# Performance work log

Measured on AMD Instinct MI355X. Metric: run time of the kernel, lower is better.

The kernel has to match this reference:

```python
import jax, jax.numpy as jnp
import numpy as np
import math

B, L = 32, 1000
N_CHAR, EMB, D_MODEL, N_HEADS, PRED_HS, N_OUT = 256, 512, 512, 8, 512, 8
D_HEAD = D_MODEL // N_HEADS


def _pos_encoding(seq_len, d_model, dtype=jnp.float32):
    pos = jnp.arange(seq_len, dtype=dtype)[:, None]                      # [L,1]
    div = jnp.exp(jnp.arange(0, d_model, 2, dtype=dtype) * (-math.log(10000.0) / d_model))
    pe = jnp.zeros((seq_len, d_model), dtype=dtype)
    pe = pe.at[:, 0::2].set(jnp.sin(pos * div))
    pe = pe.at[:, 1::2].set(jnp.cos(pos * div))
    return pe                                                            # [L,D]


def setup_inputs() -> dict:
    key = jax.random.key(0)
    ks = jax.random.split(key, 12)
    def xavier(k, shape):
        fan_in, fan_out = shape[1], shape[0]
        lim = math.sqrt(6.0 / (fan_in + fan_out))
        return jax.random.uniform(k, shape, jnp.float32, -lim, lim)
    data = jax.random.randint(ks[0], (B, L), 0, N_CHAR, dtype=jnp.int64)
    lengths = jnp.clip(jax.random.randint(ks[1], (B,), 0, L, dtype=jnp.int64), 1, L)
    emb = jax.random.normal(ks[2], (N_CHAR, EMB), jnp.float32) * math.sqrt(2.0 / (N_CHAR + EMB))
    return {
        'data': data,
        'lengths': lengths,
        'emb': emb,
        'Wq': xavier(ks[3], (D_MODEL, EMB)), 'bq': jnp.zeros((D_MODEL,), jnp.float32),
        'Wk': xavier(ks[4], (D_MODEL, EMB)), 'bk': jnp.zeros((D_MODEL,), jnp.float32),
        'Wv': xavier(ks[5], (D_MODEL, EMB)), 'bv': jnp.zeros((D_MODEL,), jnp.float32),
        'W1': xavier(ks[6], (PRED_HS, D_MODEL)), 'b1': jnp.full((PRED_HS,), 0.01, jnp.float32),
        'W2': xavier(ks[7], (N_OUT, PRED_HS)), 'b2': jnp.full((N_OUT,), 0.01, jnp.float32),
    }


def reference(data, lengths, emb, Wq, bq, Wk, bk, Wv, bv, W1, b1, W2, b2):
    bs, seq = data.shape
    x = emb[data]                                              # [B,L,E]
    x = x + _pos_encoding(seq, x.shape[-1], x.dtype)[None]     # positional encoding
    # q/k/v projections -> [B,L,H,dh]
    q = (x @ Wq.T + bq).reshape(bs, seq, N_HEADS, D_HEAD)
    k = (x @ Wk.T + bk).reshape(bs, seq, N_HEADS, D_HEAD)
    v = (x @ Wv.T + bv).reshape(bs, seq, N_HEADS, D_HEAD)
    scale = 1.0 / math.sqrt(D_HEAD)
    score = jnp.einsum('bqhd,bkhd->bhqk', q, k) * scale        # [B,H,L,L]
    causal = jnp.tril(jnp.ones((seq, seq), dtype=bool))        # True = keep
    score = jnp.where(causal[None, None], score, -jnp.inf)
    attn = jax.nn.softmax(score, axis=-1)
    ctx = jnp.einsum('bhqk,bkhd->bqhd', attn, v).reshape(bs, seq, D_MODEL)
    # take hidden state at last valid position per sequence
    ctx_last = jnp.take_along_axis(ctx, (lengths - 1)[:, None, None].astype(jnp.int32), axis=1)[:, 0]  # [B,D]
    h = jax.nn.leaky_relu(ctx_last @ W1.T + b1)                # pred layer 1
    out = jax.nn.relu(h @ W2.T + b2)                           # [B,8]
    out = jnp.mean(out, axis=-1)                               # [B]
    return jax.nn.leaky_relu(out)
```

## Files before the change

### kernel.cpp

```cpp
#include <hip/hip_runtime.h>
#include <math.h>

#define BATCH   32
#define LSEQ    1000
#define LPAD    1024
#define NHEADS  8
#define DHEAD   64

__device__ __forceinline__ unsigned short f2bf(float f) {
  unsigned u = __builtin_bit_cast(unsigned, f);
  u += 0x7fffu + ((u >> 16) & 1u);
  return (unsigned short)(u >> 16);
}
__device__ __forceinline__ float bf2f(unsigned short h) {
  return __builtin_bit_cast(float, ((unsigned)h) << 16);
}

__global__ __launch_bounds__(256) void build_x_kernel(
    const int* __restrict__ data, const int* __restrict__ lengths,
    const float* __restrict__ emb, unsigned short* __restrict__ X) {
  int t    = threadIdx.x;
  int row  = blockIdx.x * 4 + (t >> 6);
  int b    = row / 1000;
  int j    = row - b * 1000;
  int p    = lengths[b] - 1;
  if (j > p) return;
  int lane = t & 63;
  int e0   = lane * 8;
  int tok  = data[row];
  const float* ev = emb + (size_t)tok * 512 + e0;
  float4 a = *(const float4*)(ev);
  float4 c = *(const float4*)(ev + 4);
  float vals[8] = {a.x, a.y, a.z, a.w, c.x, c.y, c.z, c.w};
  #pragma unroll
  for (int i = 0; i < 8; i += 2) {
    int e = e0 + i;
    float dv  = __expf((float)e * (-9.210340371976184f / 512.0f));
    float arg = (float)j * dv;
    vals[i]     += __sinf(arg);
    vals[i + 1] += __cosf(arg);
  }
  unsigned w0 = (unsigned)f2bf(vals[0]) | ((unsigned)f2bf(vals[1]) << 16);
  unsigned w1 = (unsigned)f2bf(vals[2]) | ((unsigned)f2bf(vals[3]) << 16);
  unsigned w2 = (unsigned)f2bf(vals[4]) | ((unsigned)f2bf(vals[5]) << 16);
  unsigned w3 = (unsigned)f2bf(vals[6]) | ((unsigned)f2bf(vals[7]) << 16);
  uint4 pk; pk.x = w0; pk.y = w1; pk.z = w2; pk.w = w3;
  *(uint4*)(X + ((size_t)(b * LPAD + j)) * 512 + e0) = pk;
}

__global__ __launch_bounds__(256) void qfold_kernel(
    const unsigned short* __restrict__ X, const int* __restrict__ lengths,
    const float* __restrict__ Wq, const float* __restrict__ bq,
    const float* __restrict__ Wk, const float* __restrict__ bk,
    float* __restrict__ wfold, float* __restrict__ bias_dot) {
  int h = blockIdx.x, b = blockIdx.y;
  int p = lengths[b] - 1;
  int t = threadIdx.x;
  __shared__ float xs[512];
  __shared__ float red[256];
  __shared__ float qs[64];
  const unsigned short* xr = X + ((size_t)(b * LPAD + p)) * 512;
  xs[t]       = bf2f(xr[t]);
  xs[t + 256] = bf2f(xr[t + 256]);
  __syncthreads();
  int col = h * 64 + (t & 63);
  int kp  = t >> 6;
  {
    const float* wr = Wq + (size_t)col * 512 + kp * 128;
    const float* xp = xs + kp * 128;
    float a = 0.0f;
    for (int e = 0; e < 128; e += 4) {
      float4 wv = *(const float4*)(wr + e);
      a += wv.x * xp[e] + wv.y * xp[e + 1] + wv.z * xp[e + 2] + wv.w * xp[e + 3];
    }
    red[t] = a;
  }
  __syncthreads();
  if (t < 64) {
    float qval = (red[t] + red[t + 64] + red[t + 128] + red[t + 192]
                  + bq[h * 64 + t]) * 0.125f;
    qs[t] = qval;
    float bd = qval * bk[h * 64 + t];
    #pragma unroll
    for (int o = 32; o > 0; o >>= 1) bd += __shfl_xor(bd, o, 64);
    if (t == 0) bias_dot[b * NHEADS + h] = bd;
  }
  __syncthreads();
  float a0 = 0.0f, a1 = 0.0f;
  const float* wkb = Wk + (size_t)(h * 64) * 512;
  for (int d = 0; d < 64; ++d) {
    float qd = qs[d];
    a0 += qd * wkb[d * 512 + t];
    a1 += qd * wkb[d * 512 + t + 256];
  }
  size_t wb = ((size_t)(b * NHEADS + h)) * 512;
  wfold[wb + t]       = a0;
  wfold[wb + t + 256] = a1;
}

__global__ __launch_bounds__(256) void score_kernel(
    const unsigned short* __restrict__ X, const float* __restrict__ wfold,
    const float* __restrict__ bias_dot, const int* __restrict__ lengths,
    float* __restrict__ scores) {
  int b = blockIdx.y;
  int n_keys = lengths[b];
  int row0 = blockIdx.x * 16;
  if (row0 >= n_keys) return;
  int t = threadIdx.x;
  int w = t >> 6, lane = t & 63;
  float wf[8][8];
  float bd[8];
  size_t wbase = ((size_t)b * NHEADS) * 512 + lane * 8;
  #pragma unroll
  for (int h = 0; h < 8; ++h) {
    float4 u0 = *(const float4*)(wfold + wbase + h * 512);
    float4 u1 = *(const float4*)(wfold + wbase + h * 512 + 4);
    wf[h][0] = u0.x; wf[h][1] = u0.y; wf[h][2] = u0.z; wf[h][3] = u0.w;
    wf[h][4] = u1.x; wf[h][5] = u1.y; wf[h][6] = u1.z; wf[h][7] = u1.w;
    bd[h] = bias_dot[b * NHEADS + h];
  }
  #pragma unroll
  for (int r = 0; r < 4; ++r) {
    int j = row0 + r * 4 + w;
    if (j >= n_keys) continue;
    const unsigned short* xr = X + ((size_t)(b * LPAD + j)) * 512 + lane * 8;
    uint4 u = *(const uint4*)xr;
    unsigned uu[4] = {u.x, u.y, u.z, u.w};
    float xf[8];
    #pragma unroll
    for (int wi = 0; wi < 4; ++wi) {
      xf[wi * 2]     = __builtin_bit_cast(float, uu[wi] << 16);
      xf[wi * 2 + 1] = __builtin_bit_cast(float, uu[wi] & 0xffff0000u);
    }
    #pragma unroll
    for (int h = 0; h < 8; ++h) {
      float s = xf[0] * wf[h][0] + xf[1] * wf[h][1] + xf[2] * wf[h][2]
              + xf[3] * wf[h][3] + xf[4] * wf[h][4] + xf[5] * wf[h][5]
              + xf[6] * wf[h][6] + xf[7] * wf[h][7];
      #pragma unroll
      for (int o = 1; o < 64; o <<= 1) s += __shfl_xor(s, o, 64);
      if (lane == 0)
        scores[((size_t)(b * NHEADS + h)) * LPAD + j] = s + bd[h];
    }
  }
}

__global__ __launch_bounds__(256) void softmax_kernel(
    const float* __restrict__ scores, const int* __restrict__ lengths,
    float* __restrict__ probs, float* __restrict__ sums) {
  int h = blockIdx.x, b = blockIdx.y;
  int n = lengths[b];
  int t = threadIdx.x;
  __shared__ float red[4];
  size_t base = ((size_t)(b * NHEADS + h)) * LPAD;
  float lm = -INFINITY;
  for (int j = t; j < n; j += 256) lm = fmaxf(lm, scores[base + j]);
  #pragma unroll
  for (int o = 32; o > 0; o >>= 1) lm = fmaxf(lm, __shfl_xor(lm, o, 64));
  if ((t & 63) == 0) red[t >> 6] = lm;
  __syncthreads();
  float gmax = fmaxf(fmaxf(red[0], red[1]), fmaxf(red[2], red[3]));
  __syncthreads();
  float ls = 0.0f;
  for (int j = t; j < n; j += 256) {
    float e = __expf(scores[base + j] - gmax);
    probs[base + j] = e;
    ls += e;
  }
  #pragma unroll
  for (int o = 32; o > 0; o >>= 1) ls += __shfl_xor(ls, o, 64);
  if ((t & 63) == 0) red[t >> 6] = ls;
  __syncthreads();
  if (t == 0) sums[b * NHEADS + h] = red[0] + red[1] + red[2] + red[3];
}

__global__ __launch_bounds__(256) void ypass_kernel(
    const unsigned short* __restrict__ X, const float* __restrict__ probs,
    const int* __restrict__ lengths, float* __restrict__ y_part) {
  int jc = blockIdx.x, b = blockIdx.y;
  int n_keys = lengths[b];
  int j0 = jc * 256;
  if (j0 >= n_keys) return;
  int cnt = min(256, n_keys - j0);
  int t = threadIdx.x;
  __shared__ float pl[8][256];
  #pragma unroll
  for (int h = 0; h < 8; ++h)
    pl[h][t] = (t < cnt) ? probs[((size_t)(b * NHEADS + h)) * LPAD + j0 + t] : 0.0f;
  __syncthreads();
  int w = t >> 6, lane = t & 63;
  float acc[8][8];
  #pragma unroll
  for (int h = 0; h < 8; ++h)
    #pragma unroll
    for (int i = 0; i < 8; ++i) acc[h][i] = 0.0f;
  for (int jj = w; jj < cnt; jj += 4) {
    const unsigned short* xr = X + ((size_t)(b * LPAD + j0 + jj)) * 512 + lane * 8;
    uint4 u = *(const uint4*)xr;
    unsigned uu[4] = {u.x, u.y, u.z, u.w};
    float xf[8];
    #pragma unroll
    for (int wi = 0; wi < 4; ++wi) {
      xf[wi * 2]     = __builtin_bit_cast(float, uu[wi] << 16);
      xf[wi * 2 + 1] = __builtin_bit_cast(float, uu[wi] & 0xffff0000u);
    }
    #pragma unroll
    for (int h = 0; h < 8; ++h) {
      float pj = pl[h][jj];
      #pragma unroll
      for (int i = 0; i < 8; ++i) acc[h][i] += pj * xf[i];
    }
  }
  size_t sb = (((size_t)(b * 4 + jc)) * 4 + w) * (8 * 512) + lane * 8;
  #pragma unroll
  for (int h = 0; h < 8; ++h)
    #pragma unroll
    for (int i = 0; i < 8; ++i) y_part[sb + h * 512 + i] = acc[h][i];
}

__global__ __launch_bounds__(256) void ctx_kernel(
    const float* __restrict__ y_part, const float* __restrict__ sums,
    const int* __restrict__ lengths, const float* __restrict__ Wv,
    const float* __restrict__ bv, float* __restrict__ ctx) {
  int h = blockIdx.x, b = blockIdx.y;
  int t = threadIdx.x;
  __shared__ float ys[512];
  __shared__ float red[256];
  int n_keys = lengths[b];
  int nc = (n_keys + 255) >> 8;
  float inv = 1.0f / sums[b * NHEADS + h];
  float s0 = 0.0f, s1 = 0.0f;
  for (int jc = 0; jc < nc; ++jc) {
    #pragma unroll
    for (int w = 0; w < 4; ++w) {
      size_t sb = (((size_t)(b * 4 + jc)) * 4 + w) * (8 * 512) + h * 512;
      s0 += y_part[sb + t];
      s1 += y_part[sb + t + 256];
    }
  }
  ys[t]       = s0 * inv;
  ys[t + 256] = s1 * inv;
  __syncthreads();
  int col = h * 64 + (t & 63);
  int kp  = t >> 6;
  const float* wr = Wv + (size_t)col * 512 + kp * 128;
  const float* xp = ys + kp * 128;
  float a = 0.0f;
  for (int e = 0; e < 128; e += 4) {
    float4 wv = *(const float4*)(wr + e);
    a += wv.x * xp[e] + wv.y * xp[e + 1] + wv.z * xp[e + 2] + wv.w * xp[e + 3];
  }
  red[t] = a;
  __syncthreads();
  if (t < 64)
    ctx[b * 512 + h * 64 + t] =
        red[t] + red[t + 64] + red[t + 128] + red[t + 192] + bv[h * 64 + t];
}

__global__ __launch_bounds__(256) void mlp1_kernel(
    const float* __restrict__ ctx, const float* __restrict__ W1,
    const float* __restrict__ b1, float* __restrict__ hs) {
  int chunk = blockIdx.x, b = blockIdx.y;
  int t = threadIdx.x;
  __shared__ float xs[512];
  __shared__ float red[256];
  xs[t]       = ctx[b * 512 + t];
  xs[t + 256] = ctx[b * 512 + t + 256];
  __syncthreads();
  int col = chunk * 64 + (t & 63);
  int kp  = t >> 6;
  const float* wr = W1 + (size_t)col * 512 + kp * 128;
  const float* xp = xs + kp * 128;
  float a = 0.0f;
  for (int e = 0; e < 128; e += 4) {
    float4 wv = *(const float4*)(wr + e);
    a += wv.x * xp[e] + wv.y * xp[e + 1] + wv.z * xp[e + 2] + wv.w * xp[e + 3];
  }
  red[t] = a;
  __syncthreads();
  if (t < 64) {
    float v = red[t] + red[t + 64] + red[t + 128] + red[t + 192] + b1[chunk * 64 + t];
    hs[b * 512 + chunk * 64 + t] = (v > 0.0f) ? v : 0.01f * v;
  }
}

__global__ __launch_bounds__(256) void mlp2_kernel(
    const float* __restrict__ hs, const float* __restrict__ W2,
    const float* __restrict__ b2, float* __restrict__ out) {
  int b = blockIdx.x, t = threadIdx.x;
  __shared__ float o8[8];
  int j = t >> 5, sub = t & 31;
  const float* hr  = hs + (size_t)b * 512;
  const float* w2r = W2 + (size_t)j * 512;
  float part = 0.0f;
  for (int e = sub * 16; e < sub * 16 + 16; e += 4) {
    float4 wv = *(const float4*)(w2r + e);
    float4 hv = *(const float4*)(hr + e);
    part += wv.x * hv.x + wv.y * hv.y + wv.z * hv.z + wv.w * hv.w;
  }
  #pragma unroll
  for (int o = 16; o > 0; o >>= 1) part += __shfl_xor(part, o, 64);
  if (sub == 0) o8[j] = fmaxf(part + b2[j], 0.0f);
  __syncthreads();
  if (t == 0) {
    float m = 0.0f;
    #pragma unroll
    for (int i = 0; i < 8; ++i) m += o8[i];
    m *= 0.125f;
    out[b] = (m > 0.0f) ? m : 0.01f * m;
  }
}

extern "C" void kernel_launch(void* const* d_in, const int* in_sizes, int n_in,
                              void* d_out, int out_size, void* d_ws, size_t ws_size,
                              hipStream_t stream) {
  const int*   data    = (const int*)d_in[0];
  const int*   lengths = (const int*)d_in[1];
  const float* emb     = (const float*)d_in[2];
  const float* Wq      = (const float*)d_in[3];
  const float* bq      = (const float*)d_in[4];
  const float* Wk      = (const float*)d_in[5];
  const float* bk      = (const float*)d_in[6];
  const float* Wv      = (const float*)d_in[7];
  const float* bv      = (const float*)d_in[8];
  const float* W1      = (const float*)d_in[9];
  const float* b1      = (const float*)d_in[10];
  const float* W2      = (const float*)d_in[11];
  const float* b2      = (const float*)d_in[12];
  float* out = (float*)d_out;

  char* ws = (char*)d_ws;
  unsigned short* X = (unsigned short*)(ws);
  float* wfold      = (float*)(ws + 33554432);
  float* bias_dot   = (float*)(ws + 34078720);
  float* scores     = (float*)(ws + 34079744);
  float* probs      = (float*)(ws + 35128320);
  float* sums       = (float*)(ws + 36176896);
  float* y_part     = (float*)(ws + 36177920);
  float* ctx        = (float*)(ws + 44566528);
  float* hs         = (float*)(ws + 44632064);

  build_x_kernel<<<8000, 256, 0, stream>>>(data, lengths, emb, X);
  dim3 g2(NHEADS, BATCH);
  qfold_kernel<<<g2, 256, 0, stream>>>(X, lengths, Wq, bq, Wk, bk, wfold, bias_dot);
  dim3 g3(63, BATCH);
  score_kernel<<<g3, 256, 0, stream>>>(X, wfold, bias_dot, lengths, scores);
  dim3 g4(NHEADS, BATCH);
  softmax_kernel<<<g4, 256, 0, stream>>>(scores, lengths, probs, sums);
  dim3 g5(4, BATCH);
  ypass_kernel<<<g5, 256, 0, stream>>>(X, probs, lengths, y_part);
  dim3 g6(NHEADS, BATCH);
  ctx_kernel<<<g6, 256, 0, stream>>>(y_part, sums, lengths, Wv, bv, ctx);
  dim3 g7(8, BATCH);
  mlp1_kernel<<<g7, 256, 0, stream>>>(ctx, W1, b1, hs);
  mlp2_kernel<<<BATCH, 256, 0, stream>>>(hs, W2, b2, out);
}
```

Measured before the change: 155.8 us.

## Factor scores into token and position dot tables, drop materialized X

Removes the bf16 X buffer. Because x = emb[tok] + pe[j], each score splits into a per-token dot (256 tokens) plus a per-position dot (1000 positions) against the folded query vector. These are precomputed once into an MD table, so attention becomes gathers plus softmax in one kernel. The ypass rebuilds x on the fly from emb and sin/cos, and the Wv/W1/W2 tail is merged into one kernel per batch. This cuts the large write and re-read of X and several launches. The cost is recomputing transcendentals in ypass and serializing the tail GEMVs per block.

After: 237.4 us. +52.4%, slower.

```diff
diff --git a/kernel.cpp b/kernel.cpp
--- a/kernel.cpp
+++ b/kernel.cpp
@@ -3,65 +3,33 @@
 
 #define BATCH   32
 #define LSEQ    1000
-#define LPAD    1024
 #define NHEADS  8
 #define DHEAD   64
-
-__device__ __forceinline__ unsigned short f2bf(float f) {
-  unsigned u = __builtin_bit_cast(unsigned, f);
-  u += 0x7fffu + ((u >> 16) & 1u);
-  return (unsigned short)(u >> 16);
-}
-__device__ __forceinline__ float bf2f(unsigned short h) {
-  return __builtin_bit_cast(float, ((unsigned)h) << 16);
-}
-
-__global__ __launch_bounds__(256) void build_x_kernel(
+#define PE_C    (-9.210340371976184f / 512.0f)
+
+__device__ __forceinline__ float pe_val(int j, int e) {
+  int ef = e & ~1;
+  float dv  = __expf((float)ef * PE_C);
+  float arg = (float)j * dv;
+  return (e & 1) ? __cosf(arg) : __sinf(arg);
+}
+
+__global__ __launch_bounds__(256) void qfold_kernel(
     const int* __restrict__ data, const int* __restrict__ lengths,
-    const float* __restrict__ emb, unsigned short* __restrict__ X) {
-  int t    = threadIdx.x;
-  int row  = blockIdx.x * 4 + (t >> 6);
-  int b    = row / 1000;
-  int j    = row - b * 1000;
-  int p    = lengths[b] - 1;
-  if (j > p) return;
-  int lane = t & 63;
-  int e0   = lane * 8;
-  int tok  = data[row];
-  const float* ev = emb + (size_t)tok * 512 + e0;
-  float4 a = *(const float4*)(ev);
-  float4 c = *(const float4*)(ev + 4);
-  float vals[8] = {a.x, a.y, a.z, a.w, c.x, c.y, c.z, c.w};
-  #pragma unroll
-  for (int i = 0; i < 8; i += 2) {
-    int e = e0 + i;
-    float dv  = __expf((float)e * (-9.210340371976184f / 512.0f));
-    float arg = (float)j * dv;
-    vals[i]     += __sinf(arg);
-    vals[i + 1] += __cosf(arg);
-  }
-  unsigned w0 = (unsigned)f2bf(vals[0]) | ((unsigned)f2bf(vals[1]) << 16);
-  unsigned w1 = (unsigned)f2bf(vals[2]) | ((unsigned)f2bf(vals[3]) << 16);
-  unsigned w2 = (unsigned)f2bf(vals[4]) | ((unsigned)f2bf(vals[5]) << 16);
-  unsigned w3 = (unsigned)f2bf(vals[6]) | ((unsigned)f2bf(vals[7]) << 16);
-  uint4 pk; pk.x = w0; pk.y = w1; pk.z = w2; pk.w = w3;
-  *(uint4*)(X + ((size_t)(b * LPAD + j)) * 512 + e0) = pk;
-}
-
-__global__ __launch_bounds__(256) void qfold_kernel(
-    const unsigned short* __restrict__ X, const int* __restrict__ lengths,
+    const float* __restrict__ emb,
     const float* __restrict__ Wq, const float* __restrict__ bq,
     const float* __restrict__ Wk, const float* __restrict__ bk,
-    float* __restrict__ wfold, float* __restrict__ bias_dot) {
+    float* __restrict__ wfT4, float* __restrict__ bias_dot) {
   int h = blockIdx.x, b = blockIdx.y;
   int p = lengths[b] - 1;
   int t = threadIdx.x;
   __shared__ float xs[512];
   __shared__ float red[256];
   __shared__ float qs[64];
-  const unsigned short* xr = X + ((size_t)(b * LPAD + p)) * 512;
-  xs[t]       = bf2f(xr[t]);
-  xs[t + 256] = bf2f(xr[t + 256]);
+  int tok = data[b * LSEQ + p];
+  const float* er = emb + (size_t)tok * 512;
+  xs[t]       = er[t]       + pe_val(p, t);
+  xs[t + 256] = er[t + 256] + pe_val(p, t + 256);
   __syncthreads();
   int col = h * 64 + (t & 63);
   int kp  = t >> 6;
@@ -93,210 +61,203 @@
     a0 += qd * wkb[d * 512 + t];
     a1 += qd * wkb[d * 512 + t + 256];
   }
-  size_t wb = ((size_t)(b * NHEADS + h)) * 512;
-  wfold[wb + t]       = a0;
-  wfold[wb + t + 256] = a1;
-}
-
-__global__ __launch_bounds__(256) void score_kernel(
-    const unsigned short* __restrict__ X, const float* __restrict__ wfold,
-    const float* __restrict__ bias_dot, const int* __restrict__ lengths,
-    float* __restrict__ scores) {
-  int b = blockIdx.y;
-  int n_keys = lengths[b];
-  int row0 = blockIdx.x * 16;
-  if (row0 >= n_keys) return;
-  int t = threadIdx.x;
-  int w = t >> 6, lane = t & 63;
-  float wf[8][8];
-  float bd[8];
-  size_t wbase = ((size_t)b * NHEADS) * 512 + lane * 8;
-  #pragma unroll
-  for (int h = 0; h < 8; ++h) {
-    float4 u0 = *(const float4*)(wfold + wbase + h * 512);
-    float4 u1 = *(const float4*)(wfold + wbase + h * 512 + 4);
-    wf[h][0] = u0.x; wf[h][1] = u0.y; wf[h][2] = u0.z; wf[h][3] = u0.w;
-    wf[h][4] = u1.x; wf[h][5] = u1.y; wf[h][6] = u1.z; wf[h][7] = u1.w;
-    bd[h] = bias_dot[b * NHEADS + h];
-  }
-  #pragma unroll
-  for (int r = 0; r < 4; ++r) {
-    int j = row0 + r * 4 + w;
-    if (j >= n_keys) continue;
-    const unsigned short* xr = X + ((size_t)(b * LPAD + j)) * 512 + lane * 8;
-    uint4 u = *(const uint4*)xr;
-    unsigned uu[4] = {u.x, u.y, u.z, u.w};
-    float xf[8];
-    #pragma unroll
-    for (int wi = 0; wi < 4; ++wi) {
-      xf[wi * 2]     = __builtin_bit_cast(float, uu[wi] << 16);
-      xf[wi * 2 + 1] = __builtin_bit_cast(float, uu[wi] & 0xffff0000u);
-    }
-    #pragma unroll
-    for (int h = 0; h < 8; ++h) {
-      float s = xf[0] * wf[h][0] + xf[1] * wf[h][1] + xf[2] * wf[h][2]
-              + xf[3] * wf[h][3] + xf[4] * wf[h][4] + xf[5] * wf[h][5]
-              + xf[6] * wf[h][6] + xf[7] * wf[h][7];
-      #pragma unroll
-      for (int o = 1; o < 64; o <<= 1) s += __shfl_xor(s, o, 64);
-      if (lane == 0)
-        scores[((size_t)(b * NHEADS + h)) * LPAD + j] = s + bd[h];
-    }
-  }
-}
-
-__global__ __launch_bounds__(256) void softmax_kernel(
-    const float* __restrict__ scores, const int* __restrict__ lengths,
+  int bh = b * NHEADS + h;
+  int e1 = t, e2 = t + 256;
+  wfT4[(e1 >> 2) * 1024 + bh * 4 + (e1 & 3)] = a0;
+  wfT4[(e2 >> 2) * 1024 + bh * 4 + (e2 & 3)] = a1;
+}
+
+__global__ __launch_bounds__(256) void foldmd_kernel(
+    const float* __restrict__ emb, const float* __restrict__ wfT4,
+    float* __restrict__ MD) {
+  __shared__ float rows[8][512];
+  int t  = threadIdx.x;
+  int rr = t >> 5;
+  int e0 = (t & 31) * 16;
+  int rg = blockIdx.x * 8 + rr;
+  if (rg < 256) {
+    const float* er = emb + (size_t)rg * 512 + e0;
+    #pragma unroll
+    for (int i = 0; i < 16; i += 4) {
+      float4 v = *(const float4*)(er + i);
+      rows[rr][e0 + i]     = v.x; rows[rr][e0 + i + 1] = v.y;
+      rows[rr][e0 + i + 2] = v.z; rows[rr][e0 + i + 3] = v.w;
+    }
+  } else {
+    int j = rg - 256;
+    #pragma unroll
+    for (int i = 0; i < 16; i += 2) {
+      int e = e0 + i;
+      float dv  = __expf((float)e * PE_C);
+      float arg = (float)j * dv;
+      rows[rr][e]     = __sinf(arg);
+      rows[rr][e + 1] = __cosf(arg);
+    }
+  }
+  __syncthreads();
+  float acc[8] = {0, 0, 0, 0, 0, 0, 0, 0};
+  for (int g = 0; g < 128; ++g) {
+    float4 w4 = *(const float4*)(wfT4 + g * 1024 + t * 4);
+    #pragma unroll
+    for (int r = 0; r < 8; ++r)
+      acc[r] += rows[r][4 * g] * w4.x + rows[r][4 * g + 1] * w4.y
+              + rows[r][4 * g + 2] * w4.z + rows[r][4 * g + 3] * w4.w;
+  }
+  #pragma unroll
+  for (int r = 0; r < 8; ++r)
+    MD[(size_t)(blockIdx.x * 8 + r) * 256 + t] = acc[r];
+}
+
+__global__ __launch_bounds__(256) void attn_kernel(
+    const int* __restrict__ data, const int* __restrict__ lengths,
+    const float* __restrict__ MD, const float* __restrict__ bias_dot,
     float* __restrict__ probs, float* __restrict__ sums) {
   int h = blockIdx.x, b = blockIdx.y;
+  int bh = b * NHEADS + h;
   int n = lengths[b];
   int t = threadIdx.x;
-  __shared__ float red[4];
-  size_t base = ((size_t)(b * NHEADS + h)) * LPAD;
-  float lm = -INFINITY;
-  for (int j = t; j < n; j += 256) lm = fmaxf(lm, scores[base + j]);
-  #pragma unroll
-  for (int o = 32; o > 0; o >>= 1) lm = fmaxf(lm, __shfl_xor(lm, o, 64));
-  if ((t & 63) == 0) red[t >> 6] = lm;
-  __syncthreads();
-  float gmax = fmaxf(fmaxf(red[0], red[1]), fmaxf(red[2], red[3]));
-  __syncthreads();
+  __shared__ float redm[4];
+  __shared__ float redsum[4];
+  const float* Edot = MD;
+  const float* Pdot = MD + 256 * 256;
+  float bd = bias_dot[bh];
+  float sreg[4];
+  int   nit = 0;
+  float lmax = -INFINITY;
+  for (int j = t; j < n; j += 256) {
+    int tok = data[b * LSEQ + j];
+    float s = Edot[tok * 256 + bh] + Pdot[(size_t)j * 256 + bh] + bd;
+    sreg[nit++] = s;
+    lmax = fmaxf(lmax, s);
+  }
+  #pragma unroll
+  for (int o = 32; o > 0; o >>= 1) lmax = fmaxf(lmax, __shfl_xor(lmax, o, 64));
+  if ((t & 63) == 0) redm[t >> 6] = lmax;
+  __syncthreads();
+  float gmax = fmaxf(fmaxf(redm[0], redm[1]), fmaxf(redm[2], redm[3]));
   float ls = 0.0f;
-  for (int j = t; j < n; j += 256) {
-    float e = __expf(scores[base + j] - gmax);
-    probs[base + j] = e;
-    ls += e;
+  {
+    int it = 0;
+    for (int j = t; j < n; j += 256) {
+      float e = __expf(sreg[it++] - gmax);
+      probs[(size_t)bh * 1024 + j] = e;
+      ls += e;
+    }
   }
   #pragma unroll
   for (int o = 32; o > 0; o >>= 1) ls += __shfl_xor(ls, o, 64);
-  if ((t & 63) == 0) red[t >> 6] = ls;
-  __syncthreads();
-  if (t == 0) sums[b * NHEADS + h] = red[0] + red[1] + red[2] + red[3];
+  if ((t & 63) == 0) redsum[t >> 6] = ls;
+  __syncthreads();
+  if (t == 0) sums[bh] = redsum[0] + redsum[1] + redsum[2] + redsum[3];
 }
 
 __global__ __launch_bounds__(256) void ypass_kernel(
-    const unsigned short* __restrict__ X, const float* __restrict__ probs,
-    const int* __restrict__ lengths, float* __restrict__ y_part) {
+    const int* __restrict__ data, const int* __restrict__ lengths,
+    const float* __restrict__ emb, const float* __restrict__ probs,
+    float* __restrict__ y_part) {
   int jc = blockIdx.x, b = blockIdx.y;
-  int n_keys = lengths[b];
-  int j0 = jc * 256;
-  if (j0 >= n_keys) return;
-  int cnt = min(256, n_keys - j0);
+  int n = lengths[b];
+  int j0 = jc * 125;
+  if (j0 >= n) return;
+  int cnt = min(125, n - j0);
   int t = threadIdx.x;
-  __shared__ float pl[8][256];
-  #pragma unroll
-  for (int h = 0; h < 8; ++h)
-    pl[h][t] = (t < cnt) ? probs[((size_t)(b * NHEADS + h)) * LPAD + j0 + t] : 0.0f;
+  __shared__ float pl[128][8];
+  __shared__ int   tk[128];
+  if (t < cnt) {
+    tk[t] = data[b * LSEQ + j0 + t];
+    #pragma unroll
+    for (int h = 0; h < 8; ++h)
+      pl[t][h] = probs[(size_t)(b * NHEADS + h) * 1024 + j0 + t];
+  }
   __syncthreads();
   int w = t >> 6, lane = t & 63;
-  float acc[8][8];
-  #pragma unroll
-  for (int h = 0; h < 8; ++h)
-    #pragma unroll
-    for (int i = 0; i < 8; ++i) acc[h][i] = 0.0f;
-  for (int jj = w; jj < cnt; jj += 4) {
-    const unsigned short* xr = X + ((size_t)(b * LPAD + j0 + jj)) * 512 + lane * 8;
-    uint4 u = *(const uint4*)xr;
-    unsigned uu[4] = {u.x, u.y, u.z, u.w};
-    float xf[8];
-    #pragma unroll
-    for (int wi = 0; wi < 4; ++wi) {
-      xf[wi * 2]     = __builtin_bit_cast(float, uu[wi] << 16);
-      xf[wi * 2 + 1] = __builtin_bit_cast(float, uu[wi] & 0xffff0000u);
-    }
+  int e0 = w * 128 + lane * 2;
+  float dv = __expf((float)e0 * PE_C);
+  float acc0[8] = {0,0,0,0,0,0,0,0};
+  float acc1[8] = {0,0,0,0,0,0,0,0};
+  for (int jj = 0; jj < cnt; ++jj) {
+    int tok = tk[jj];
+    float2 ev = *(const float2*)(emb + (size_t)tok * 512 + e0);
+    float arg = (float)(j0 + jj) * dv;
+    float x0 = ev.x + __sinf(arg);
+    float x1 = ev.y + __cosf(arg);
     #pragma unroll
     for (int h = 0; h < 8; ++h) {
-      float pj = pl[h][jj];
-      #pragma unroll
-      for (int i = 0; i < 8; ++i) acc[h][i] += pj * xf[i];
-    }
-  }
-  size_t sb = (((size_t)(b * 4 + jc)) * 4 + w) * (8 * 512) + lane * 8;
-  #pragma unroll
-  for (int h = 0; h < 8; ++h)
-    #pragma unroll
-    for (int i = 0; i < 8; ++i) y_part[sb + h * 512 + i] = acc[h][i];
-}
-
-__global__ __launch_bounds__(256) void ctx_kernel(
-    const float* __restrict__ y_part, const float* __restrict__ sums,
-    const int* __restrict__ lengths, const float* __restrict__ Wv,
-    const float* __restrict__ bv, float* __restrict__ ctx) {
-  int h = blockIdx.x, b = blockIdx.y;
+      float pj = pl[jj][h];
+      acc0[h] += pj * x0;
+      acc1[h] += pj * x1;
+    }
+  }
+  size_t base = (size_t)(b * 8 + jc) * 4096 + e0;
+  #pragma unroll
+  for (int h = 0; h < 8; ++h) {
+    float2 o; o.x = acc0[h]; o.y = acc1[h];
+    *(float2*)(y_part + base + h * 512) = o;
+  }
+}
+
+__global__ __launch_bounds__(256) void tail_kernel(
+    const int* __restrict__ lengths, const float* __restrict__ y_part,
+    const float* __restrict__ sums,
+    const float* __restrict__ Wv, const float* __restrict__ bv,
+    const float* __restrict__ W1, const float* __restrict__ b1,
+    const float* __restrict__ W2, const float* __restrict__ b2,
+    float* __restrict__ out) {
+  int b = blockIdx.x;
   int t = threadIdx.x;
-  __shared__ float ys[512];
-  __shared__ float red[256];
-  int n_keys = lengths[b];
-  int nc = (n_keys + 255) >> 8;
-  float inv = 1.0f / sums[b * NHEADS + h];
-  float s0 = 0.0f, s1 = 0.0f;
-  for (int jc = 0; jc < nc; ++jc) {
-    #pragma unroll
-    for (int w = 0; w < 4; ++w) {
-      size_t sb = (((size_t)(b * 4 + jc)) * 4 + w) * (8 * 512) + h * 512;
-      s0 += y_part[sb + t];
-      s1 += y_part[sb + t + 256];
-    }
-  }
-  ys[t]       = s0 * inv;
-  ys[t + 256] = s1 * inv;
-  __syncthreads();
-  int col = h * 64 + (t & 63);
-  int kp  = t >> 6;
-  const float* wr = Wv + (size_t)col * 512 + kp * 128;
-  const float* xp = ys + kp * 128;
-  float a = 0.0f;
-  for (int e = 0; e < 128; e += 4) {
-    float4 wv = *(const float4*)(wr + e);
-    a += wv.x * xp[e] + wv.y * xp[e + 1] + wv.z * xp[e + 2] + wv.w * xp[e + 3];
-  }
-  red[t] = a;
-  __syncthreads();
-  if (t < 64)
-    ctx[b * 512 + h * 64 + t] =
-        red[t] + red[t + 64] + red[t + 128] + red[t + 192] + bv[h * 64 + t];
-}
-
-__global__ __launch_bounds__(256) void mlp1_kernel(
-    const float* __restrict__ ctx, const float* __restrict__ W1,
-    const float* __restrict__ b1, float* __restrict__ hs) {
-  int chunk = blockIdx.x, b = blockIdx.y;
-  int t = threadIdx.x;
-  __shared__ float xs[512];
-  __shared__ float red[256];
-  xs[t]       = ctx[b * 512 + t];
-  xs[t + 256] = ctx[b * 512 + t + 256];
-  __syncthreads();
-  int col = chunk * 64 + (t & 63);
-  int kp  = t >> 6;
-  const float* wr = W1 + (size_t)col * 512 + kp * 128;
-  const float* xp = xs + kp * 128;
-  float a = 0.0f;
-  for (int e = 0; e < 128; e += 4) {
-    float4 wv = *(const float4*)(wr + e);
-    a += wv.x * xp[e] + wv.y * xp[e + 1] + wv.z * xp[e + 2] + wv.w * xp[e + 3];
-  }
-  red[t] = a;
-  __syncthreads();
-  if (t < 64) {
-    float v = red[t] + red[t + 64] + red[t + 128] + red[t + 192] + b1[chunk * 64 + t];
-    hs[b * 512 + chunk * 64 + t] = (v > 0.0f) ? v : 0.01f * v;
-  }
-}
-
-__global__ __launch_bounds__(256) void mlp2_kernel(
-    const float* __restrict__ hs, const float* __restrict__ W2,
-    const float* __restrict__ b2, float* __restrict__ out) {
-  int b = blockIdx.x, t = threadIdx.x;
+  __shared__ float ys[4096];
+  __shared__ float cx[512];
+  __shared__ float hsd[512];
+  __shared__ float invl[8];
   __shared__ float o8[8];
+  int n = lengths[b];
+  int nc = (n + 124) / 125;
+  if (t < 8) invl[t] = 1.0f / sums[b * NHEADS + t];
+  __syncthreads();
+  #pragma unroll
+  for (int i = 0; i < 16; ++i) {
+    int idx = t + i * 256;
+    float s = 0.0f;
+    for (int jc = 0; jc < nc; ++jc)
+      s += y_part[(size_t)(b * 8 + jc) * 4096 + idx];
+    ys[idx] = s * invl[idx >> 9];
+  }
+  __syncthreads();
+  #pragma unroll
+  for (int cc = 0; cc < 2; ++cc) {
+    int col = t + cc * 256;
+    const float* wr = Wv + (size_t)col * 512;
+    const float* yp = ys + ((col >> 6) << 9);
+    float a = 0.0f;
+    for (int e = 0; e < 512; e += 4) {
+      float4 wv4 = *(const float4*)(wr + e);
+      float4 yv  = *(const float4*)(yp + e);
+      a += wv4.x * yv.x + wv4.y * yv.y + wv4.z * yv.z + wv4.w * yv.w;
+    }
+    cx[col] = a + bv[col];
+  }
+  __syncthreads();
+  #pragma unroll
+  for (int cc = 0; cc < 2; ++cc) {
+    int col = t + cc * 256;
+    const float* wr = W1 + (size_t)col * 512;
+    float a = 0.0f;
+    for (int e = 0; e < 512; e += 4) {
+      float4 wv4 = *(const float4*)(wr + e);
+      float4 yv  = *(const float4*)(cx + e);
+      a += wv4.x * yv.x + wv4.y * yv.y + wv4.z * yv.z + wv4.w * yv.w;
+    }
+    a += b1[col];
+    hsd[col] = (a > 0.0f) ? a : 0.01f * a;
+  }
+  __syncthreads();
   int j = t >> 5, sub = t & 31;
-  const float* hr  = hs + (size_t)b * 512;
   const float* w2r = W2 + (size_t)j * 512;
   float part = 0.0f;
   for (int e = sub * 16; e < sub * 16 + 16; e += 4) {
-    float4 wv = *(const float4*)(w2r + e);
-    float4 hv = *(const float4*)(hr + e);
-    part += wv.x * hv.x + wv.y * hv.y + wv.z * hv.z + wv.w * hv.w;
+    float4 wv4 = *(const float4*)(w2r + e);
+    part += wv4.x * hsd[e] + wv4.y * hsd[e + 1]
+          + wv4.z * hsd[e + 2] + wv4.w * hsd[e + 3];
   }
   #pragma unroll
   for (int o = 16; o > 0; o >>= 1) part += __shfl_xor(part, o, 64);
@@ -330,28 +291,21 @@
   float* out = (float*)d_out;
 
   char* ws = (char*)d_ws;
-  unsigned short* X = (unsigned short*)(ws);
-  float* wfold      = (float*)(ws + 33554432);
-  float* bias_dot   = (float*)(ws + 34078720);
-  float* scores     = (float*)(ws + 34079744);
-  float* probs      = (float*)(ws + 35128320);
-  float* sums       = (float*)(ws + 36176896);
-  float* y_part     = (float*)(ws + 36177920);
-  float* ctx        = (float*)(ws + 44566528);
-  float* hs         = (float*)(ws + 44632064);
-
-  build_x_kernel<<<8000, 256, 0, stream>>>(data, lengths, emb, X);
-  dim3 g2(NHEADS, BATCH);
-  qfold_kernel<<<g2, 256, 0, stream>>>(X, lengths, Wq, bq, Wk, bk, wfold, bias_dot);
-  dim3 g3(63, BATCH);
-  score_kernel<<<g3, 256, 0, stream>>>(X, wfold, bias_dot, lengths, scores);
-  dim3 g4(NHEADS, BATCH);
-  softmax_kernel<<<g4, 256, 0, stream>>>(scores, lengths, probs, sums);
-  dim3 g5(4, BATCH);
-  ypass_kernel<<<g5, 256, 0, stream>>>(X, probs, lengths, y_part);
-  dim3 g6(NHEADS, BATCH);
-  ctx_kernel<<<g6, 256, 0, stream>>>(y_part, sums, lengths, Wv, bv, ctx);
-  dim3 g7(8, BATCH);
-  mlp1_kernel<<<g7, 256, 0, stream>>>(ctx, W1, b1, hs);
-  mlp2_kernel<<<BATCH, 256, 0, stream>>>(hs, W2, b2, out);
-}
+  float* wfT4     = (float*)(ws);
+  float* MD       = (float*)(ws + 524288);
+  float* bias_dot = (float*)(ws + 1810432);
+  float* probs    = (float*)(ws + 1811456);
+  float* sums     = (float*)(ws + 2860032);
+  float* y_part   = (float*)(ws + 2861056);
+
+  dim3 g1(NHEADS, BATCH);
+  qfold_kernel<<<g1, 256, 0, stream>>>(data, lengths, emb, Wq, bq, Wk, bk,
+                                       wfT4, bias_dot);
+  foldmd_kernel<<<157, 256, 0, stream>>>(emb, wfT4, MD);
+  dim3 g3(NHEADS, BATCH);
+  attn_kernel<<<g3, 256, 0, stream>>>(data, lengths, MD, bias_dot, probs, sums);
+  dim3 g4(8, BATCH);
+  ypass_kernel<<<g4, 256, 0, stream>>>(data, lengths, emb, probs, y_part);
+  tail_kernel<<<BATCH, 256, 0, stream>>>(lengths, y_part, sums, Wv, bv,
+                                         W1, b1, W2, b2, out);
+}
```
